# Kernel tuning notes

Measured on AMD Instinct MI355X. Metric: run time of the kernel, lower is better.

Reference implementation:

```python
import jax, jax.numpy as jnp
import numpy as np

B, T, C, D = 4, 4096, 1024, 64

def setup_inputs() -> dict:
    key = jax.random.key(0)
    k1, k2, k3, k4 = jax.random.split(key, 4)
    return {
        "x": jax.random.normal(k1, (B, T, C), dtype=jnp.float32),
        "Wq": jax.random.normal(k2, (C, D), dtype=jnp.float32) * (C ** -0.5),
        "Wk": jax.random.normal(k3, (C, D), dtype=jnp.float32) * (C ** -0.5),
        "Wv": jax.random.normal(k4, (C, D), dtype=jnp.float32) * (C ** -0.5),
    }

def reference(x, Wq, Wk, Wv):
    # Single-head causal self-attention (context defaults to x; dropout p=0 -> identity)
    T_ = x.shape[1]
    Q = jnp.einsum('btc,cd->btd', x, Wq)
    K = jnp.einsum('btc,cd->btd', x, Wk)
    V = jnp.einsum('btc,cd->btd', x, Wv)
    scores = jnp.einsum('btd,bsd->bts', Q, K) / jnp.sqrt(jnp.float32(K.shape[-1]))
    causal = jnp.tril(jnp.ones((T_, T_), dtype=bool))  # [T, T]
    scores = jnp.where(causal, scores, -jnp.inf)
    attn = jax.nn.softmax(scores, axis=-1)
    out = jnp.einsum('bts,bsd->btd', attn, V)
    return out
```

## Files before the change

### kernel.cpp

```cpp
#include <hip/hip_runtime.h>

typedef short bf16x8 __attribute__((ext_vector_type(8)));
typedef float f32x4 __attribute__((ext_vector_type(4)));
typedef float f32x16 __attribute__((ext_vector_type(16)));
typedef unsigned short u16;
typedef unsigned int u32;

#define MFMA_BF16 __builtin_amdgcn_mfma_f32_16x16x32_bf16
#define MFMA32 __builtin_amdgcn_mfma_f32_32x32x16_bf16

static __device__ __forceinline__ u16 f2bf(float f) {
  union { float f; unsigned u; } v; v.f = f;
  return (u16)((v.u + 0x7FFFu + ((v.u >> 16) & 1u)) >> 16);
}
static __device__ __forceinline__ u32 cvtpk(float lo, float hi) {
  u32 r;
  asm("v_cvt_pk_bf16_f32 %0, %1, %2" : "=v"(r) : "v"(lo), "v"(hi));
  return r;
}
static __device__ __forceinline__ bf16x8 cvt8(uint4 p, uint4 q) {
  union { u32 w[4]; bf16x8 b; } r;
  r.w[0] = cvtpk(__uint_as_float(p.x), __uint_as_float(p.y));
  r.w[1] = cvtpk(__uint_as_float(p.z), __uint_as_float(p.w));
  r.w[2] = cvtpk(__uint_as_float(q.x), __uint_as_float(q.y));
  r.w[3] = cvtpk(__uint_as_float(q.z), __uint_as_float(q.w));
  return r.b;
}
static __device__ __forceinline__ float xhalf(float x) { return __shfl_xor(x, 32); }
static __device__ __forceinline__ u32 xhalfu(u32 x) { return (u32)__shfl_xor((int)x, 32); }

static __device__ __forceinline__ void gload16(const void* g, void* l) {
  __builtin_amdgcn_global_load_lds(
      (const __attribute__((address_space(1))) u32*)g,
      (__attribute__((address_space(3))) u32*)l, 16, 0, 0);
}

__global__ __launch_bounds__(256) void wt_kernel(const float* __restrict__ Wq,
                                                 const float* __restrict__ Wk,
                                                 const float* __restrict__ Wv,
                                                 u16* __restrict__ Wt) {
  const int nrow = blockIdx.x;
  const int m = nrow >> 6, n = nrow & 63;
  const float* W = (m == 0) ? Wq : ((m == 1) ? Wk : Wv);
  const float s = (m == 0) ? 0.125f * 1.44269504f : 1.0f;
  for (int k = threadIdx.x; k < 1024; k += 256)
    Wt[(size_t)nrow * 1024 + k] = f2bf(W[(size_t)k * 64 + n] * s);
}

__global__ __launch_bounds__(256) void qkv6(const float* __restrict__ x,
                                            const u16* __restrict__ Wt,
                                            u16* __restrict__ Qb,
                                            u16* __restrict__ Kb,
                                            u16* __restrict__ Vt) {
  __shared__ __align__(16) char sh[2][32 * 1024];
  const int w = threadIdx.x >> 6, l = threadIdx.x & 63;
  const int lane16 = l & 15, laneHi = l >> 4;
  const int r0 = blockIdx.x * 32;
  const int nt0 = w * 3;

  const f32x4 fzero = {0.f, 0.f, 0.f, 0.f};
  f32x4 acc0 = fzero, acc1 = fzero, acc2 = fzero;
  f32x4 acc3 = fzero, acc4 = fzero, acc5 = fzero;

  auto stage = [&](int buf, int s) {
    char* base = &sh[buf][0];
    const int k0 = s * 64;
    if (w < 3) {
#pragma unroll
      for (int ii = 0; ii < 8; ++ii) {
        const int nt = w * 4 + (ii >> 1), kh = ii & 1;
        const u16* g = Wt + (size_t)(nt * 16 + lane16) * 1024 + k0 + kh * 32 + laneHi * 8;
        gload16(g, base + (nt * 2 + kh) * 1024);
      }
    } else {
#pragma unroll
      for (int ii = 0; ii < 8; ++ii) {
        const int m = ii >> 2, kh = (ii >> 1) & 1, p = ii & 1;
        const float* g = x + (size_t)(r0 + m * 16 + lane16) * 1024 + k0 + kh * 32 + laneHi * 8 + p * 4;
        gload16(g, base + (24 + ii) * 1024);
      }
    }
  };

  auto comp = [&](int buf) {
    const char* base = &sh[buf][0] + (size_t)l * 16;
    bf16x8 b00 = *(const bf16x8*)(base + ((nt0 + 0) * 2 + 0) * 1024);
    bf16x8 b01 = *(const bf16x8*)(base + ((nt0 + 0) * 2 + 1) * 1024);
    bf16x8 b10 = *(const bf16x8*)(base + ((nt0 + 1) * 2 + 0) * 1024);
    bf16x8 b11 = *(const bf16x8*)(base + ((nt0 + 1) * 2 + 1) * 1024);
    bf16x8 b20 = *(const bf16x8*)(base + ((nt0 + 2) * 2 + 0) * 1024);
    bf16x8 b21 = *(const bf16x8*)(base + ((nt0 + 2) * 2 + 1) * 1024);
    uint4 x00a = *(const uint4*)(base + 24 * 1024);
    uint4 x00b = *(const uint4*)(base + 25 * 1024);
    uint4 x01a = *(const uint4*)(base + 26 * 1024);
    uint4 x01b = *(const uint4*)(base + 27 * 1024);
    uint4 x10a = *(const uint4*)(base + 28 * 1024);
    uint4 x10b = *(const uint4*)(base + 29 * 1024);
    uint4 x11a = *(const uint4*)(base + 30 * 1024);
    uint4 x11b = *(const uint4*)(base + 31 * 1024);
    bf16x8 a00 = cvt8(x00a, x00b);
    bf16x8 a01 = cvt8(x01a, x01b);
    bf16x8 a10 = cvt8(x10a, x10b);
    bf16x8 a11 = cvt8(x11a, x11b);
    acc0 = MFMA_BF16(a00, b00, acc0, 0, 0, 0);
    acc0 = MFMA_BF16(a01, b01, acc0, 0, 0, 0);
    acc1 = MFMA_BF16(a00, b10, acc1, 0, 0, 0);
    acc1 = MFMA_BF16(a01, b11, acc1, 0, 0, 0);
    acc2 = MFMA_BF16(a00, b20, acc2, 0, 0, 0);
    acc2 = MFMA_BF16(a01, b21, acc2, 0, 0, 0);
    acc3 = MFMA_BF16(a10, b00, acc3, 0, 0, 0);
    acc3 = MFMA_BF16(a11, b01, acc3, 0, 0, 0);
    acc4 = MFMA_BF16(a10, b10, acc4, 0, 0, 0);
    acc4 = MFMA_BF16(a11, b11, acc4, 0, 0, 0);
    acc5 = MFMA_BF16(a10, b20, acc5, 0, 0, 0);
    acc5 = MFMA_BF16(a11, b21, acc5, 0, 0, 0);
  };

  stage(0, 0);
  __syncthreads();
#pragma unroll 1
  for (int s = 0; s < 16; ++s) {
    if (s + 1 < 16) stage((s + 1) & 1, s + 1);
    comp(s & 1);
    __syncthreads();
  }

#define ST(AC, m, i)                                                        \
  {                                                                         \
    const int nt = nt0 + (i);                                               \
    if (nt < 4) {                                                           \
      _Pragma("unroll")                                                     \
      for (int r = 0; r < 4; ++r)                                           \
        Qb[(size_t)(r0 + (m) * 16 + laneHi * 4 + r) * 64 + nt * 16 + lane16] = f2bf(AC[r]); \
    } else if (nt < 8) {                                                    \
      _Pragma("unroll")                                                     \
      for (int r = 0; r < 4; ++r)                                           \
        Kb[(size_t)(r0 + (m) * 16 + laneHi * 4 + r) * 64 + (nt - 4) * 16 + lane16] = f2bf(AC[r]); \
    } else {                                                                \
      const int d = (nt - 8) * 16 + lane16;                                 \
      uint2 v;                                                              \
      v.x = cvtpk(AC[0], AC[1]);                                            \
      v.y = cvtpk(AC[2], AC[3]);                                            \
      *(uint2*)(Vt + ((size_t)(r0 >> 5) * 64 + d) * 32 + (m) * 16 + laneHi * 4) = v; \
    }                                                                       \
  }

  ST(acc0, 0, 0) ST(acc1, 0, 1) ST(acc2, 0, 2)
  ST(acc3, 1, 0) ST(acc4, 1, 1) ST(acc5, 1, 2)
}

__global__ __launch_bounds__(512) void attn12(const u16* __restrict__ Qb,
                                              const u16* __restrict__ Kb,
                                              const u16* __restrict__ Vt,
                                              float* __restrict__ out) {
  __shared__ float shC[4][64][37];
  __shared__ __align__(16) float shT[32][68];

  const int tid = threadIdx.x, w = tid >> 6, l = tid & 63;
  const int q = l & 31, hi = l >> 5;
  const bool isHi = hi != 0;
  const int b = blockIdx.x & 3;
  const int p_ = blockIdx.x >> 2;
  const int tA = (p_ < 32) ? p_ : (95 - p_);
  const int tB = tA + 64;
  const int q0A = tA * 32, q0B = tB * 32, bT = b * 4096;

  const u16* qpA = Qb + (size_t)(bT + q0A + q) * 64 + 8 * hi;
  const bf16x8 qA0 = *(const bf16x8*)(qpA);
  const bf16x8 qA1 = *(const bf16x8*)(qpA + 16);
  const bf16x8 qA2 = *(const bf16x8*)(qpA + 32);
  const bf16x8 qA3 = *(const bf16x8*)(qpA + 48);
  const u16* qpB = Qb + (size_t)(bT + q0B + q) * 64 + 8 * hi;
  const bf16x8 qB0 = *(const bf16x8*)(qpB);
  const bf16x8 qB1 = *(const bf16x8*)(qpB + 16);
  const bf16x8 qB2 = *(const bf16x8*)(qpB + 32);
  const bf16x8 qB3 = *(const bf16x8*)(qpB + 48);

  const int n = tB + 1;
  const int s = (n * w) >> 3, e = (n * (w + 1)) >> 3;

  f32x16 oA0 = {}, oA1 = {}, oB0 = {}, oB1 = {};
  float mA = -INFINITY, lA = 0.f, mB = -INFINITY, lB = 0.f;

  bf16x8 kA[4], vA[4], kB[4], vB[4];

  auto loadKV = [&](bf16x8 (&kf)[4], bf16x8 (&vf)[4], int u) {
    const int k0 = bT + u * 32;
    const u16* kp = Kb + (size_t)(k0 + q) * 64 + 8 * hi;
#pragma unroll
    for (int kc = 0; kc < 4; ++kc) kf[kc] = *(const bf16x8*)(kp + kc * 16);
    const u16* vbase = Vt + (size_t)(b * 128 + u) * 2048;
#pragma unroll
    for (int dt = 0; dt < 2; ++dt)
#pragma unroll
      for (int c = 0; c < 2; ++c)
        vf[dt * 2 + c] = *(const bf16x8*)(vbase + (dt * 32 + q) * 32 + c * 16 + 8 * hi);
  };

  auto step = [&](bf16x8 (&kf)[4], bf16x8 (&vf)[4], int u, int tdiag,
                  const bf16x8& qf0, const bf16x8& qf1, const bf16x8& qf2, const bf16x8& qf3,
                  float& m, float& lsum, f32x16& o0, f32x16& o1) {
    f32x16 sc = {};
    __builtin_amdgcn_s_setprio(1);
    sc = MFMA32(kf[0], qf0, sc, 0, 0, 0);
    sc = MFMA32(kf[1], qf1, sc, 0, 0, 0);
    sc = MFMA32(kf[2], qf2, sc, 0, 0, 0);
    sc = MFMA32(kf[3], qf3, sc, 0, 0, 0);
    __builtin_amdgcn_s_setprio(0);

    if (u == tdiag) {
#pragma unroll
      for (int r = 0; r < 16; ++r) {
        const int key = (r & 3) + 8 * (r >> 2) + 4 * hi;
        if (key > q) sc[r] = -INFINITY;
      }
    }

    float pm = sc[0];
#pragma unroll
    for (int r = 1; r < 16; ++r) pm = fmaxf(pm, sc[r]);
    pm = fmaxf(pm, xhalf(pm));

    if (!__all(pm <= m + 8.f)) {
      const float mn = fmaxf(m, pm);
      const float al = exp2f(fmaxf(m - mn, -80.f));
#pragma unroll
      for (int r = 0; r < 16; ++r) { o0[r] *= al; o1[r] *= al; }
      lsum *= al;
      m = mn;
    }

    float p[16];
    float rs = 0.f;
#pragma unroll
    for (int r = 0; r < 16; ++r) { p[r] = exp2f(sc[r] - m); rs += p[r]; }
    rs += xhalf(rs);
    lsum += rs;

    u32 wl0 = cvtpk(p[0], p[1]),  wl1 = cvtpk(p[2], p[3]);
    u32 wh0 = cvtpk(p[4], p[5]),  wh1 = cvtpk(p[6], p[7]);
    u32 yl0 = cvtpk(p[8], p[9]),  yl1 = cvtpk(p[10], p[11]);
    u32 yh0 = cvtpk(p[12], p[13]), yh1 = cvtpk(p[14], p[15]);
    u32 sl0 = xhalfu(wl0), sl1 = xhalfu(wl1);
    u32 sh0 = xhalfu(wh0), sh1 = xhalfu(wh1);
    u32 tl0 = xhalfu(yl0), tl1 = xhalfu(yl1);
    u32 th0 = xhalfu(yh0), th1 = xhalfu(yh1);
    union { u32 w4[4]; bf16x8 v; } pf0, pf1;
    pf0.w4[0] = isHi ? sh0 : wl0;
    pf0.w4[1] = isHi ? sh1 : wl1;
    pf0.w4[2] = isHi ? wh0 : sl0;
    pf0.w4[3] = isHi ? wh1 : sl1;
    pf1.w4[0] = isHi ? th0 : yl0;
    pf1.w4[1] = isHi ? th1 : yl1;
    pf1.w4[2] = isHi ? yh0 : tl0;
    pf1.w4[3] = isHi ? yh1 : tl1;

    __builtin_amdgcn_s_setprio(1);
    o0 = MFMA32(vf[0], pf0.v, o0, 0, 0, 0);
    o0 = MFMA32(vf[1], pf1.v, o0, 0, 0, 0);
    o1 = MFMA32(vf[2], pf0.v, o1, 0, 0, 0);
    o1 = MFMA32(vf[3], pf1.v, o1, 0, 0, 0);
    __builtin_amdgcn_s_setprio(0);
  };

  auto computeU = [&](bf16x8 (&kf)[4], bf16x8 (&vf)[4], int u) {
    if (u <= tA) step(kf, vf, u, tA, qA0, qA1, qA2, qA3, mA, lA, oA0, oA1);
    step(kf, vf, u, tB, qB0, qB1, qB2, qB3, mB, lB, oB0, oB1);
  };

  int u = s;
  if (u < e) loadKV(kA, vA, u);
#pragma unroll 1
  while (u < e) {
    if (u + 1 < e) loadKV(kB, vB, u + 1);
    computeU(kA, vA, u);
    ++u;
    if (u >= e) break;
    if (u + 1 < e) loadKV(kA, vA, u + 1);
    computeU(kB, vB, u);
    ++u;
  }

#pragma unroll 1
  for (int pass = 0; pass < 2; ++pass) {
    float m = pass ? mB : mA, lsum = pass ? lB : lA;
    f32x16 o0 = pass ? oB0 : oA0, o1 = pass ? oB1 : oA1;
    const int q0 = pass ? q0B : q0A;

    auto publish = [&](int slot) {
      float* dst = &shC[slot][l][0];
      dst[0] = m; dst[1] = lsum;
#pragma unroll
      for (int r = 0; r < 16; ++r) { dst[2 + r] = o0[r]; dst[18 + r] = o1[r]; }
    };
    auto merge = [&](int slot) {
      const float* src = &shC[slot][l][0];
      const float pm = src[0], pl = src[1];
      const float mn = fmaxf(m, pm);
      const float aS = exp2f(fmaxf(m - mn, -80.f));
      const float aP = exp2f(fmaxf(pm - mn, -80.f));
      m = mn;
      lsum = lsum * aS + pl * aP;
#pragma unroll
      for (int r = 0; r < 16; ++r) {
        o0[r] = o0[r] * aS + src[2 + r] * aP;
        o1[r] = o1[r] * aS + src[18 + r] * aP;
      }
    };

    if (w >= 4) publish(w - 4);
    __syncthreads();
    if (w < 4) merge(w);
    __syncthreads();
    if (w >= 1 && w < 4) publish(w - 1);
    __syncthreads();
    if (w == 0) {
      merge(0); merge(1); merge(2);
      const float inv = 1.0f / lsum;
#pragma unroll
      for (int r = 0; r < 16; ++r) {
        const int d = (r & 3) + 8 * (r >> 2) + 4 * hi;
        shT[q][d] = o0[r] * inv;
        shT[q][32 + d] = o1[r] * inv;
      }
      __asm volatile("s_waitcnt lgkmcnt(0)" ::: "memory");
#pragma unroll
      for (int it = 0; it < 8; ++it) {
        const int row = it * 4 + (l >> 4);
        const int c4 = (l & 15) * 4;
        float4 v = *(const float4*)&shT[row][c4];
        *(float4*)(out + (size_t)(bT + q0 + row) * 64 + c4) = v;
      }
    }
    __syncthreads();
  }
}

extern "C" void kernel_launch(void* const* d_in, const int* in_sizes, int n_in,
                              void* d_out, int out_size, void* d_ws, size_t ws_size,
                              hipStream_t stream) {
  const float* x  = (const float*)d_in[0];
  const float* Wq = (const float*)d_in[1];
  const float* Wk = (const float*)d_in[2];
  const float* Wv = (const float*)d_in[3];
  float* out = (float*)d_out;

  char* ws = (char*)d_ws;
  u16* Wt = (u16*)ws;
  u16* Qb = (u16*)(ws + 393216);
  u16* Kb = (u16*)(ws + 393216 + 2097152);
  u16* Vt = (u16*)(ws + 393216 + 2 * 2097152);

  wt_kernel<<<192, 256, 0, stream>>>(Wq, Wk, Wv, Wt);
  qkv6<<<512, 256, 0, stream>>>(x, Wt, Qb, Kb, Vt);
  attn12<<<256, 512, 0, stream>>>(Qb, Kb, Vt, out);
}
```

Baseline: 88.49 us.

## Pair complementary query tiles and stride KV tiles across waves

Each block now handles query tiles tp and 127-tp instead of tA and tA+64, so every block carries the same causal work. Within a block, the eight waves take KV tiles round-robin (stride 8) instead of contiguous chunks. This balances which waves hit the tA cutoff and the diagonal tile. The row max and row sum are also rewritten as tree reductions to shorten the dependency chains. Strided access may cost some KV locality, and the cross-wave merge still runs as before.

After: 78.57 us. 11.2% less time.

```diff
diff --git a/kernel.cpp b/kernel.cpp
--- a/kernel.cpp
+++ b/kernel.cpp
@@ -149,7 +149,7 @@
   ST(acc3, 1, 0) ST(acc4, 1, 1) ST(acc5, 1, 2)
 }
 
-__global__ __launch_bounds__(512) void attn12(const u16* __restrict__ Qb,
+__global__ __launch_bounds__(512) void attn13(const u16* __restrict__ Qb,
                                               const u16* __restrict__ Kb,
                                               const u16* __restrict__ Vt,
                                               float* __restrict__ out) {
@@ -160,9 +160,8 @@
   const int q = l & 31, hi = l >> 5;
   const bool isHi = hi != 0;
   const int b = blockIdx.x & 3;
-  const int p_ = blockIdx.x >> 2;
-  const int tA = (p_ < 32) ? p_ : (95 - p_);
-  const int tB = tA + 64;
+  const int tp = blockIdx.x >> 2;
+  const int tA = tp, tB = 127 - tp;
   const int q0A = tA * 32, q0B = tB * 32, bT = b * 4096;
 
   const u16* qpA = Qb + (size_t)(bT + q0A + q) * 64 + 8 * hi;
@@ -176,13 +175,12 @@
   const bf16x8 qB2 = *(const bf16x8*)(qpB + 32);
   const bf16x8 qB3 = *(const bf16x8*)(qpB + 48);
 
-  const int n = tB + 1;
-  const int s = (n * w) >> 3, e = (n * (w + 1)) >> 3;
+  const int nu = tB + 1;
 
   f32x16 oA0 = {}, oA1 = {}, oB0 = {}, oB1 = {};
   float mA = -INFINITY, lA = 0.f, mB = -INFINITY, lB = 0.f;
 
-  bf16x8 kA[4], vA[4], kB[4], vB[4];
+  bf16x8 k1[4], v1[4], k2[4], v2[4];
 
   auto loadKV = [&](bf16x8 (&kf)[4], bf16x8 (&vf)[4], int u) {
     const int k0 = bT + u * 32;
@@ -216,9 +214,12 @@
       }
     }
 
-    float pm = sc[0];
-#pragma unroll
-    for (int r = 1; r < 16; ++r) pm = fmaxf(pm, sc[r]);
+    float t8[8];
+#pragma unroll
+    for (int r = 0; r < 8; ++r) t8[r] = fmaxf(sc[r], sc[r + 8]);
+    float t4a = fmaxf(t8[0], t8[1]), t4b = fmaxf(t8[2], t8[3]);
+    float t4c = fmaxf(t8[4], t8[5]), t4d = fmaxf(t8[6], t8[7]);
+    float pm = fmaxf(fmaxf(t4a, t4b), fmaxf(t4c, t4d));
     pm = fmaxf(pm, xhalf(pm));
 
     if (!__all(pm <= m + 8.f)) {
@@ -231,9 +232,14 @@
     }
 
     float p[16];
-    float rs = 0.f;
-#pragma unroll
-    for (int r = 0; r < 16; ++r) { p[r] = exp2f(sc[r] - m); rs += p[r]; }
+#pragma unroll
+    for (int r = 0; r < 16; ++r) p[r] = exp2f(sc[r] - m);
+    float s8[8];
+#pragma unroll
+    for (int r = 0; r < 8; ++r) s8[r] = p[r] + p[r + 8];
+    float s4a = s8[0] + s8[1], s4b = s8[2] + s8[3];
+    float s4c = s8[4] + s8[5], s4d = s8[6] + s8[7];
+    float rs = (s4a + s4b) + (s4c + s4d);
     rs += xhalf(rs);
     lsum += rs;
 
@@ -268,17 +274,17 @@
     step(kf, vf, u, tB, qB0, qB1, qB2, qB3, mB, lB, oB0, oB1);
   };
 
-  int u = s;
-  if (u < e) loadKV(kA, vA, u);
+  int u = w;
+  if (u < nu) loadKV(k1, v1, u);
 #pragma unroll 1
-  while (u < e) {
-    if (u + 1 < e) loadKV(kB, vB, u + 1);
-    computeU(kA, vA, u);
-    ++u;
-    if (u >= e) break;
-    if (u + 1 < e) loadKV(kA, vA, u + 1);
-    computeU(kB, vB, u);
-    ++u;
+  while (u < nu) {
+    if (u + 8 < nu) loadKV(k2, v2, u + 8);
+    computeU(k1, v1, u);
+    u += 8;
+    if (u >= nu) break;
+    if (u + 8 < nu) loadKV(k1, v1, u + 8);
+    computeU(k2, v2, u);
+    u += 8;
   }
 
 #pragma unroll 1
@@ -353,5 +359,5 @@
 
   wt_kernel<<<192, 256, 0, stream>>>(Wq, Wk, Wv, Wt);
   qkv6<<<512, 256, 0, stream>>>(x, Wt, Qb, Kb, Vt);
-  attn12<<<256, 512, 0, stream>>>(Qb, Kb, Vt, out);
-}
+  attn13<<<256, 512, 0, stream>>>(Qb, Kb, Vt, out);
+}
```
